# Optimization experiments

Measured on AMD Instinct MI355X. Metric: run time of the kernel, lower is better.

## Reference

```python
import jax, jax.numpy as jnp
import numpy as np

NB, T, N, C = 8, 8, 6890, 128
CLASS_NUM = 7
D_SUM = 512
PCADIM = 64
V = 7702  # garment template vertex count
EPS = 1e-5


def setup_inputs() -> dict:
    key = jax.random.key(0)
    ks = jax.random.split(key, 12)
    f = lambda k, s: jax.random.normal(k, s, dtype=jnp.float32)
    return {
        "x": f(ks[0], (NB, T, N, 3)),
        "sem_logits": f(ks[1], (NB * T, N, CLASS_NUM)),
        "feature": f(ks[2], (NB * T, C, N)),
        "garment_summary": f(ks[3], (NB, T, D_SUM)),
        "W1": f(ks[4], (128, D_SUM)) * 0.02, "b1": jnp.zeros((128,), jnp.float32),
        "g1": jnp.ones((128,), jnp.float32), "be1": jnp.zeros((128,), jnp.float32),
        "rm1": jnp.zeros((128,), jnp.float32), "rv1": jnp.ones((128,), jnp.float32),
        "W2": f(ks[5], (64, 128)) * 0.02, "b2": jnp.zeros((64,), jnp.float32),
        "g2": jnp.ones((64,), jnp.float32), "be2": jnp.zeros((64,), jnp.float32),
        "rm2": jnp.zeros((64,), jnp.float32), "rv2": jnp.ones((64,), jnp.float32),
        "W3": f(ks[6], (PCADIM, 64)) * 0.02, "b3": jnp.zeros((PCADIM,), jnp.float32),
        "pca_comp": f(ks[7], (PCADIM, V * 3)) * 0.02,
        "pca_mean": f(ks[8], (V * 3,)) * 0.02,
        "pca_scale": jnp.abs(f(ks[9], (V * 3,))) + 0.5,
        "garment_label": 1,
        "n": N // 4,
    }


def _segmentation_gather(x, sem_logits, feature, garment_label, n):
    # Vectorized form of the per-sample boolean-mask select / truncate / zero-pad loop.
    # x: [B,N,3]; feature: [B,C,N]; sem_logits: [B,N,K]
    feat = jnp.swapaxes(feature, 1, 2)                     # [B,N,C]
    labels = jnp.argmax(sem_logits, axis=2)                # [B,N] (detached in original)
    mask = labels == garment_label                         # [B,N]
    count = mask.sum(axis=1)                               # [B]
    # stable argsort puts selected (mask=True -> key False=0) indices first, in order
    order = jnp.argsort(jnp.logical_not(mask), axis=1)[:, :n]   # [B,n]
    valid = (jnp.arange(n)[None, :] < count[:, None]).astype(x.dtype)  # [B,n]
    gv = jnp.take_along_axis(x, order[:, :, None], axis=1) * valid[:, :, None]
    gf = jnp.take_along_axis(feat, order[:, :, None], axis=1) * valid[:, :, None]
    return gv, gf


def reference(x, sem_logits, feature, garment_summary, W1, b1, g1, be1, rm1, rv1,
              W2, b2, g2, be2, rm2, rv2, W3, b3, pca_comp, pca_mean, pca_scale,
              garment_label, n):
    nbatch, t = x.shape[0], x.shape[1]
    xf = x.reshape(nbatch * t, -1, 3)
    garment_v, garment_f = _segmentation_gather(xf, sem_logits, feature, garment_label, n)

    # PCAEncoder: 1x1 Conv1d over a length-1 sequence == linear layers; BN in eval mode
    def bn(h, g, be, rm, rv):
        return (h - rm) * jax.lax.rsqrt(rv + EPS) * g + be

    gs = garment_summary.max(axis=1)                       # [nbatch, 512] (max over T)
    h = jax.nn.relu(bn(gs @ W1.T + b1, g1, be1, rm1, rv1))
    h = jax.nn.relu(bn(h @ W2.T + b2, g2, be2, rm2, rv2))
    coeff = h @ W3.T + b3                                  # [nbatch, PCADIM]

    # PCA_inverse_transform
    tpose = ((coeff @ pca_comp) + pca_mean) * pca_scale
    tpose = tpose.reshape(coeff.shape[0], -1, 3)           # [nbatch, V, 3]
    return garment_v, garment_f, coeff, tpose
```

## Files before the change

kernel.cpp:

```cpp
#include <hip/hip_runtime.h>

#define NBATCH   8
#define TT       8
#define NPTS     6890
#define KCLS     7
#define CCH      128
#define BSAMP    64
#define NOUT     1722
#define DSUM     512
#define PCADIM   64
#define V3       23106
#define EPSBN    1e-5f

#define NW       108
#define PCH      64
#define LDSP     129
#define CPG      4
#define NGRP     27
#define K4B      91
#define NGATHER  (BSAMP * NGRP)

#define OFF_GV     0
#define OFF_GF     (BSAMP * NOUT * 3)
#define OFF_COEFF  (OFF_GF + BSAMP * NOUT * CCH)
#define OFF_TPOSE  (OFF_COEFF + NBATCH * PCADIM)

__global__ __launch_bounds__(256) void k0_mask(
    const float* __restrict__ logits,
    const int*   __restrict__ d_label,
    unsigned long long* __restrict__ ws_mask)
{
    const int b     = blockIdx.x / 27;
    const int chunk = blockIdx.x % 27;
    const int tid   = threadIdx.x;
    const int i     = chunk * 256 + tid;
    const int label = d_label[0];

    bool sel = false;
    if (i < NPTS) {
        const float* p = logits + ((size_t)b * NPTS + i) * KCLS;
        float best = p[0]; int bi = 0;
        #pragma unroll
        for (int k = 1; k < KCLS; ++k) {
            float v = p[k];
            if (v > best) { best = v; bi = k; }
        }
        sel = (bi == label);
    }
    const unsigned long long m = __ballot(sel);
    if ((tid & 63) == 0) {
        const int w = chunk * 4 + (tid >> 6);
        if (w < NW) ws_mask[b * NW + w] = m;
    }
}

__global__ __launch_bounds__(256) void k_scan_mlp(
    const float* __restrict__ x,
    const unsigned long long* __restrict__ ws_mask,
    float* __restrict__ gv,
    int*   __restrict__ ws_spref,
    int*   __restrict__ ws_count,
    const float* __restrict__ gsum,
    const float* __restrict__ W1, const float* __restrict__ b1,
    const float* __restrict__ g1, const float* __restrict__ be1,
    const float* __restrict__ rm1, const float* __restrict__ rv1,
    const float* __restrict__ W2, const float* __restrict__ b2,
    const float* __restrict__ g2, const float* __restrict__ be2,
    const float* __restrict__ rm2, const float* __restrict__ rv2,
    const float* __restrict__ W3, const float* __restrict__ b3,
    float* __restrict__ coeff_out, float* __restrict__ coeff_ws)
{
    const int tid = threadIdx.x;

    if (blockIdx.x < BSAMP) {
        const int b = blockIdx.x;
        __shared__ unsigned long long smask[NW];
        __shared__ int spref[NW + 1];

        if (tid < NW) smask[tid] = ws_mask[b * NW + tid];
        __syncthreads();
        if (tid == 0) {
            int run = 0;
            for (int w = 0; w < NW; ++w) { spref[w] = run; run += __popcll(smask[w]); }
            spref[NW] = run;
            ws_count[b] = run < NOUT ? run : NOUT;
        }
        __syncthreads();
        if (tid < NW) ws_spref[b * NW + tid] = spref[tid];

        const float* xb = x + (size_t)b * NPTS * 3;
        for (int i = tid; i < NPTS; i += 256) {
            const int w = i >> 6, lb6 = i & 63;
            const unsigned long long m = smask[w];
            if ((m >> lb6) & 1ull) {
                const int pos = spref[w] + __popcll(m & ((1ull << lb6) - 1ull));
                if (pos < NOUT) {
                    const size_t go = ((size_t)b * NOUT + pos) * 3;
                    gv[go + 0] = xb[(size_t)i * 3 + 0];
                    gv[go + 1] = xb[(size_t)i * 3 + 1];
                    gv[go + 2] = xb[(size_t)i * 3 + 2];
                }
            }
        }

        int cnt = spref[NW]; if (cnt > NOUT) cnt = NOUT;
        for (int j = cnt + tid; j < NOUT; j += 256) {
            float* gp = gv + ((size_t)b * NOUT + j) * 3;
            gp[0] = 0.f; gp[1] = 0.f; gp[2] = 0.f;
        }
    } else {
        const int s    = blockIdx.x - BSAMP;
        const int lane = tid & 63;
        const int wv   = tid >> 6;

        __shared__ float gs[DSUM];
        __shared__ float h1[128];
        __shared__ float h2[64];

        for (int d = tid; d < DSUM; d += 256) {
            const float* p = gsum + ((size_t)s * TT) * DSUM + d;
            float m = p[0];
            #pragma unroll
            for (int t = 1; t < TT; ++t) m = fmaxf(m, p[(size_t)t * DSUM]);
            gs[d] = m;
        }
        __syncthreads();

        for (int r = 0; r < 32; r += 2) {
            const int j0 = wv * 32 + r, j1 = j0 + 1;
            const float* w0 = W1 + (size_t)j0 * DSUM;
            const float* w1 = W1 + (size_t)j1 * DSUM;
            float pa = 0.f, pb = 0.f;
            #pragma unroll
            for (int d = lane; d < DSUM; d += 64) {
                const float gd = gs[d];
                pa = fmaf(w0[d], gd, pa);
                pb = fmaf(w1[d], gd, pb);
            }
            #pragma unroll
            for (int off = 32; off; off >>= 1) {
                pa += __shfl_xor(pa, off);
                pb += __shfl_xor(pb, off);
            }
            if (lane == 0) {
                pa += b1[j0];
                pa = (pa - rm1[j0]) * rsqrtf(rv1[j0] + EPSBN) * g1[j0] + be1[j0];
                h1[j0] = fmaxf(pa, 0.f);
                pb += b1[j1];
                pb = (pb - rm1[j1]) * rsqrtf(rv1[j1] + EPSBN) * g1[j1] + be1[j1];
                h1[j1] = fmaxf(pb, 0.f);
            }
        }
        __syncthreads();

        for (int r = 0; r < 16; ++r) {
            const int jj = wv * 16 + r;
            const float* w = W2 + (size_t)jj * 128;
            float p = w[lane] * h1[lane] + w[lane + 64] * h1[lane + 64];
            #pragma unroll
            for (int off = 32; off; off >>= 1) p += __shfl_xor(p, off);
            if (lane == 0) {
                p += b2[jj];
                p = (p - rm2[jj]) * rsqrtf(rv2[jj] + EPSBN) * g2[jj] + be2[jj];
                h2[jj] = fmaxf(p, 0.f);
            }
        }
        __syncthreads();

        for (int r = 0; r < 16; ++r) {
            const int jj = wv * 16 + r;
            float p = W3[(size_t)jj * 64 + lane] * h2[lane];
            #pragma unroll
            for (int off = 32; off; off >>= 1) p += __shfl_xor(p, off);
            if (lane == 0) {
                p += b3[jj];
                coeff_out[s * PCADIM + jj] = p;
                coeff_ws[s * PCADIM + jj]  = p;
            }
        }
    }
}

__global__ __launch_bounds__(256, 4) void k2_fused(
    const float* __restrict__ feature,
    const unsigned long long* __restrict__ ws_mask,
    const int* __restrict__ ws_spref,
    const int* __restrict__ ws_count,
    float* __restrict__ gf,
    const float* __restrict__ coeff_ws,
    const float* __restrict__ comp,
    const float* __restrict__ mean_,
    const float* __restrict__ scale_,
    float* __restrict__ tpose)
{
    __shared__ float lds[PCH * LDSP];
    __shared__ int   spos[PCH];
    __shared__ int   sel_list[PCH];
    __shared__ int   s_nsel;

    const int tid = threadIdx.x;

    if (blockIdx.x >= NGATHER) {
        float* sc = lds;
        for (int o = tid; o < NBATCH * PCADIM; o += 256) sc[o] = coeff_ws[o];
        __syncthreads();

        const int v = (blockIdx.x - NGATHER) * 256 + tid;
        if (v >= V3) return;

        float acc[NBATCH];
        #pragma unroll
        for (int s = 0; s < NBATCH; ++s) acc[s] = 0.f;
        for (int k = 0; k < PCADIM; ++k) {
            const float pv = comp[(size_t)k * V3 + v];
            #pragma unroll
            for (int s = 0; s < NBATCH; ++s)
                acc[s] = fmaf(sc[s * PCADIM + k], pv, acc[s]);
        }
        const float mn = mean_[v], scl = scale_[v];
        #pragma unroll
        for (int s = 0; s < NBATCH; ++s)
            tpose[(size_t)s * V3 + v] = (acc[s] + mn) * scl;
        return;
    }

    const int b   = blockIdx.x / NGRP;
    const int g   = blockIdx.x % NGRP;
    const int pt2 = tid & 31;
    const int cg  = tid >> 5;
    const int p0  = pt2 * 2;
    const float* fbase = feature + (size_t)b * CCH * NPTS;

    float2 rc[16], rn[16];

    {
        const int i0 = g * (CPG * PCH);
        const int il = min(PCH, NPTS - i0);
        const float* fb = fbase + i0 + p0;
        if (p0 < il) {
            #pragma unroll
            for (int it = 0; it < 16; ++it)
                rc[it] = *(const float2*)(fb + (size_t)(cg + 8 * it) * NPTS);
        } else {
            #pragma unroll
            for (int it = 0; it < 16; ++it) rc[it] = make_float2(0.f, 0.f);
        }
    }

    #pragma unroll
    for (int c = 0; c < CPG; ++c) {
        const int chunk = g * CPG + c;

        if (c + 1 < CPG) {
            const int i1 = (chunk + 1) * PCH;
            const int il = min(PCH, NPTS - i1);
            const float* fb = fbase + i1 + p0;
            if (p0 < il) {
                #pragma unroll
                for (int it = 0; it < 16; ++it)
                    rn[it] = *(const float2*)(fb + (size_t)(cg + 8 * it) * NPTS);
            } else {
                #pragma unroll
                for (int it = 0; it < 16; ++it) rn[it] = make_float2(0.f, 0.f);
            }
        }

        __syncthreads();

        #pragma unroll
        for (int it = 0; it < 16; ++it) {
            const int cch = cg + 8 * it;
            lds[p0 * LDSP + cch]       = rc[it].x;
            lds[(p0 + 1) * LDSP + cch] = rc[it].y;
        }

        if (tid < 64) {
            const unsigned long long m = ws_mask[b * NW + chunk];
            const int base = ws_spref[b * NW + chunk];
            const int sel  = (int)((m >> tid) & 1ull);
            const int pos  = base + __popcll(m & ((1ull << tid) - 1ull));
            const int sp   = (sel && pos < NOUT) ? pos : -1;
            spos[tid] = sp;
            const unsigned long long mm = __ballot(sp >= 0);
            const int before = __popcll(mm & ((1ull << tid) - 1ull));
            if (sp >= 0) sel_list[before] = tid;
            if (tid == 0) s_nsel = __popcll(mm);
        }
        __syncthreads();

        const int nsel = s_nsel;
        const int cc = tid & 127;
        for (int s = tid >> 7; s < nsel; s += 2) {
            const int p = sel_list[s];
            gf[((size_t)b * NOUT + spos[p]) * CCH + cc] = lds[p * LDSP + cc];
        }

        if (c + 1 < CPG) {
            #pragma unroll
            for (int it = 0; it < 16; ++it) rc[it] = rn[it];
        }
    }

    {
        const int cnt   = ws_count[b];
        const int tail  = NOUT - cnt;
        if (tail > 0) {
            const int share = (tail + NGRP - 1) / NGRP;
            const int r0    = cnt + g * share;
            const int r1    = min(r0 + share, NOUT);
            const int nrows = r1 - r0;
            if (nrows > 0) {
                float4* base4 = (float4*)(gf + ((size_t)b * NOUT + r0) * CCH);
                const int total = nrows * 32;
                for (int f = tid; f < total; f += 256)
                    base4[f] = make_float4(0.f, 0.f, 0.f, 0.f);
            }
        }
    }
}

extern "C" void kernel_launch(void* const* d_in, const int* in_sizes, int n_in,
                              void* d_out, int out_size, void* d_ws, size_t ws_size,
                              hipStream_t stream) {
    const float* x      = (const float*)d_in[0];
    const float* logits = (const float*)d_in[1];
    const float* feat   = (const float*)d_in[2];
    const float* gsum   = (const float*)d_in[3];
    const float* W1  = (const float*)d_in[4];
    const float* b1  = (const float*)d_in[5];
    const float* g1  = (const float*)d_in[6];
    const float* be1 = (const float*)d_in[7];
    const float* rm1 = (const float*)d_in[8];
    const float* rv1 = (const float*)d_in[9];
    const float* W2  = (const float*)d_in[10];
    const float* b2  = (const float*)d_in[11];
    const float* g2  = (const float*)d_in[12];
    const float* be2 = (const float*)d_in[13];
    const float* rm2 = (const float*)d_in[14];
    const float* rv2 = (const float*)d_in[15];
    const float* W3  = (const float*)d_in[16];
    const float* b3  = (const float*)d_in[17];
    const float* comp  = (const float*)d_in[18];
    const float* mean_ = (const float*)d_in[19];
    const float* scale_= (const float*)d_in[20];
    const int* d_label = (const int*)d_in[21];

    float* out   = (float*)d_out;
    float* gv    = out + OFF_GV;
    float* gf    = out + OFF_GF;
    float* coeff = out + OFF_COEFF;
    float* tpose = out + OFF_TPOSE;

    unsigned long long* ws_mask = (unsigned long long*)d_ws;
    int*   ws_spref = (int*)(ws_mask + BSAMP * NW);
    int*   ws_count = ws_spref + BSAMP * NW;
    float* coeff_ws = (float*)(ws_count + BSAMP);

    k0_mask   <<<BSAMP * 27,       256, 0, stream>>>(logits, d_label, ws_mask);
    k_scan_mlp<<<BSAMP + NBATCH,   256, 0, stream>>>(x, ws_mask, gv, ws_spref, ws_count,
                                                     gsum, W1, b1, g1, be1, rm1, rv1,
                                                     W2, b2, g2, be2, rm2, rv2, W3, b3,
                                                     coeff, coeff_ws);
    k2_fused  <<<NGATHER + K4B,    256, 0, stream>>>(feat, ws_mask, ws_spref, ws_count,
                                                     gf, coeff_ws, comp, mean_, scale_,
                                                     tpose);
}
```

Baseline: 100.7 us.

## Fuse mask kernel into scan kernel, regroup gather blocks, reorder block roles

The argmax/ballot mask computation moves into the per-sample scan blocks, which drops one kernel launch and the global round trip for the mask. The gather kernel now handles 6 chunks per block instead of 4, giving fewer blocks. PCA blocks are placed first in the grid, and the zero-fill of the padded tail is issued before the gather loop. The cost is that the mask work now runs on only 64 blocks instead of about 1700, which serialises logits reading inside each block.

```diff
diff --git a/kernel.cpp b/kernel.cpp
--- a/kernel.cpp
+++ b/kernel.cpp
@@ -15,8 +15,8 @@
 #define NW       108
 #define PCH      64
 #define LDSP     129
-#define CPG      4
-#define NGRP     27
+#define CPG      6
+#define NGRP     18
 #define K4B      91
 #define NGATHER  (BSAMP * NGRP)
 
@@ -25,38 +25,11 @@
 #define OFF_COEFF  (OFF_GF + BSAMP * NOUT * CCH)
 #define OFF_TPOSE  (OFF_COEFF + NBATCH * PCADIM)
 
-__global__ __launch_bounds__(256) void k0_mask(
+__global__ __launch_bounds__(256) void k_prep(
     const float* __restrict__ logits,
     const int*   __restrict__ d_label,
-    unsigned long long* __restrict__ ws_mask)
-{
-    const int b     = blockIdx.x / 27;
-    const int chunk = blockIdx.x % 27;
-    const int tid   = threadIdx.x;
-    const int i     = chunk * 256 + tid;
-    const int label = d_label[0];
-
-    bool sel = false;
-    if (i < NPTS) {
-        const float* p = logits + ((size_t)b * NPTS + i) * KCLS;
-        float best = p[0]; int bi = 0;
-        #pragma unroll
-        for (int k = 1; k < KCLS; ++k) {
-            float v = p[k];
-            if (v > best) { best = v; bi = k; }
-        }
-        sel = (bi == label);
-    }
-    const unsigned long long m = __ballot(sel);
-    if ((tid & 63) == 0) {
-        const int w = chunk * 4 + (tid >> 6);
-        if (w < NW) ws_mask[b * NW + w] = m;
-    }
-}
-
-__global__ __launch_bounds__(256) void k_scan_mlp(
     const float* __restrict__ x,
-    const unsigned long long* __restrict__ ws_mask,
+    unsigned long long* __restrict__ ws_mask,
     float* __restrict__ gv,
     int*   __restrict__ ws_spref,
     int*   __restrict__ ws_count,
@@ -74,11 +47,33 @@
 
     if (blockIdx.x < BSAMP) {
         const int b = blockIdx.x;
+        const int label = d_label[0];
         __shared__ unsigned long long smask[NW];
         __shared__ int spref[NW + 1];
 
-        if (tid < NW) smask[tid] = ws_mask[b * NW + tid];
-        __syncthreads();
+        const float* lb = logits + (size_t)b * NPTS * KCLS;
+        #pragma unroll 1
+        for (int r = 0; r < 27; ++r) {
+            const int i = r * 256 + tid;
+            bool sel = false;
+            if (i < NPTS) {
+                const float* p = lb + (size_t)i * KCLS;
+                float best = p[0]; int bi = 0;
+                #pragma unroll
+                for (int k = 1; k < KCLS; ++k) {
+                    float v = p[k];
+                    if (v > best) { best = v; bi = k; }
+                }
+                sel = (bi == label);
+            }
+            const unsigned long long m = __ballot(sel);
+            if ((tid & 63) == 0) {
+                const int w = r * 4 + (tid >> 6);
+                if (w < NW) smask[w] = m;
+            }
+        }
+        __syncthreads();
+
         if (tid == 0) {
             int run = 0;
             for (int w = 0; w < NW; ++w) { spref[w] = run; run += __popcll(smask[w]); }
@@ -86,7 +81,10 @@
             ws_count[b] = run < NOUT ? run : NOUT;
         }
         __syncthreads();
-        if (tid < NW) ws_spref[b * NW + tid] = spref[tid];
+        if (tid < NW) {
+            ws_mask [b * NW + tid] = smask[tid];
+            ws_spref[b * NW + tid] = spref[tid];
+        }
 
         const float* xb = x + (size_t)b * NPTS * 3;
         for (int i = tid; i < NPTS; i += 256) {
@@ -181,7 +179,7 @@
     }
 }
 
-__global__ __launch_bounds__(256, 4) void k2_fused(
+__global__ __launch_bounds__(256, 4) void k_gather(
     const float* __restrict__ feature,
     const unsigned long long* __restrict__ ws_mask,
     const int* __restrict__ ws_spref,
@@ -200,12 +198,12 @@
 
     const int tid = threadIdx.x;
 
-    if (blockIdx.x >= NGATHER) {
+    if (blockIdx.x < K4B) {
         float* sc = lds;
         for (int o = tid; o < NBATCH * PCADIM; o += 256) sc[o] = coeff_ws[o];
         __syncthreads();
 
-        const int v = (blockIdx.x - NGATHER) * 256 + tid;
+        const int v = blockIdx.x * 256 + tid;
         if (v >= V3) return;
 
         float acc[NBATCH];
@@ -224,8 +222,9 @@
         return;
     }
 
-    const int b   = blockIdx.x / NGRP;
-    const int g   = blockIdx.x % NGRP;
+    const int gb  = blockIdx.x - K4B;
+    const int b   = gb / NGRP;
+    const int g   = gb % NGRP;
     const int pt2 = tid & 31;
     const int cg  = tid >> 5;
     const int p0  = pt2 * 2;
@@ -244,6 +243,23 @@
         } else {
             #pragma unroll
             for (int it = 0; it < 16; ++it) rc[it] = make_float2(0.f, 0.f);
+        }
+    }
+
+    {
+        const int cnt  = ws_count[b];
+        const int tail = NOUT - cnt;
+        if (tail > 0) {
+            const int share = (tail + NGRP - 1) / NGRP;
+            const int r0    = cnt + g * share;
+            const int r1    = min(r0 + share, NOUT);
+            const int nrows = r1 - r0;
+            if (nrows > 0) {
+                float4* base4 = (float4*)(gf + ((size_t)b * NOUT + r0) * CCH);
+                const int total = nrows * 32;
+                for (int f = tid; f < total; f += 256)
+                    base4[f] = make_float4(0.f, 0.f, 0.f, 0.f);
+            }
         }
     }
 
@@ -298,23 +314,6 @@
         if (c + 1 < CPG) {
             #pragma unroll
             for (int it = 0; it < 16; ++it) rc[it] = rn[it];
-        }
-    }
-
-    {
-        const int cnt   = ws_count[b];
-        const int tail  = NOUT - cnt;
-        if (tail > 0) {
-            const int share = (tail + NGRP - 1) / NGRP;
-            const int r0    = cnt + g * share;
-            const int r1    = min(r0 + share, NOUT);
-            const int nrows = r1 - r0;
-            if (nrows > 0) {
-                float4* base4 = (float4*)(gf + ((size_t)b * NOUT + r0) * CCH);
-                const int total = nrows * 32;
-                for (int f = tid; f < total; f += 256)
-                    base4[f] = make_float4(0.f, 0.f, 0.f, 0.f);
-            }
         }
     }
 }
@@ -356,12 +355,12 @@
     int*   ws_count = ws_spref + BSAMP * NW;
     float* coeff_ws = (float*)(ws_count + BSAMP);
 
-    k0_mask   <<<BSAMP * 27,       256, 0, stream>>>(logits, d_label, ws_mask);
-    k_scan_mlp<<<BSAMP + NBATCH,   256, 0, stream>>>(x, ws_mask, gv, ws_spref, ws_count,
-                                                     gsum, W1, b1, g1, be1, rm1, rv1,
-                                                     W2, b2, g2, be2, rm2, rv2, W3, b3,
-                                                     coeff, coeff_ws);
-    k2_fused  <<<NGATHER + K4B,    256, 0, stream>>>(feat, ws_mask, ws_spref, ws_count,
-                                                     gf, coeff_ws, comp, mean_, scale_,
-                                                     tpose);
+    k_prep  <<<BSAMP + NBATCH,  256, 0, stream>>>(logits, d_label, x, ws_mask, gv,
+                                                  ws_spref, ws_count,
+                                                  gsum, W1, b1, g1, be1, rm1, rv1,
+                                                  W2, b2, g2, be2, rm2, rv2, W3, b3,
+                                                  coeff, coeff_ws);
+    k_gather<<<K4B + NGATHER,   256, 0, stream>>>(feat, ws_mask, ws_spref, ws_count,
+                                                  gf, coeff_ws, comp, mean_, scale_,
+                                                  tpose);
 }
```

Result: no change. 99.07 us (-1.6%).
